# Performance work log

Measured on AMD Instinct MI355X. Metric: run time of the kernel, lower is better.

The kernel has to match this reference:

```python
import jax, jax.numpy as jnp
import numpy as np

N, E, F, H, C = 50000, 800000, 100, 128, 40
EPS = 1e-5


def setup_inputs() -> dict:
    key = jax.random.key(0)
    ks = jax.random.split(key, 9)
    s = 0.05
    return {
        "x": jax.random.normal(ks[0], (N, F), jnp.float32),
        "nbr": jax.random.normal(ks[1], (E, F), jnp.float32),
        "seg_ids": jnp.sort(jax.random.randint(ks[2], (E,), 0, N)),
        "W1x": jax.random.normal(ks[3], (H, F), jnp.float32) * s,
        "W1n": jax.random.normal(ks[4], (H, F), jnp.float32) * s,
        "g1": jnp.ones((), jnp.float32),
        "b1": jnp.zeros((), jnp.float32),
        "W2x": jax.random.normal(ks[5], (H, H), jnp.float32) * s,
        "W2n": jax.random.normal(ks[6], (H, H), jnp.float32) * s,
        "g2": jnp.ones((), jnp.float32),
        "b2": jnp.zeros((), jnp.float32),
        "Wc": jax.random.normal(ks[7], (C, H), jnp.float32) * s,
        "bc": jnp.zeros((C,), jnp.float32),
    }


def _seg_mean(v, ids, n):
    # ragged per-node neighbor mean: segment_sum / count
    s = jax.ops.segment_sum(v, ids, num_segments=n)
    cnt = jax.ops.segment_sum(jnp.ones((v.shape[0],), v.dtype), ids, num_segments=n)
    return s / jnp.maximum(cnt, 1.0)[:, None], cnt


def _bn_relu(t, g, b):
    # BatchNorm1d(1) in training mode on [N,1,d]: scalar mean/var over all elements
    m = t.mean()
    v = jnp.mean((t - m) ** 2)
    return jax.nn.relu(g * (t - m) * jax.lax.rsqrt(v + EPS) + b)


def _seg_bn_relu(nbr, ids, cnt, g, b, n):
    # BN applied per neighbor-list tensor: scalar stats per segment (over k_i * d elems)
    d = nbr.shape[1]
    ne = jnp.maximum(cnt * d, 1.0)
    sm = jax.ops.segment_sum(nbr.sum(axis=1), ids, num_segments=n) / ne
    sq = jax.ops.segment_sum((nbr * nbr).sum(axis=1), ids, num_segments=n) / ne
    var = sq - sm * sm
    inv = jax.lax.rsqrt(var + EPS)
    xn = (nbr - sm[ids, None]) * inv[ids, None]
    return jax.nn.relu(g * xn + b)


def reference(x, nbr, seg_ids, W1x, W1n, g1, b1, W2x, W2n, g2, b2, Wc, bc):
    n = x.shape[0]
    # layer 1: FeatTrans(feat_len -> hidden)
    f, cnt = _seg_mean(nbr, seg_ids, n)          # [N,F]
    h = x @ W1x.T + f @ W1n.T                    # [N,H]
    nbr1 = nbr @ W1x.T                           # [E,H]
    # acvt1
    h = _bn_relu(h, g1, b1)
    nbr1 = _seg_bn_relu(nbr1, seg_ids, cnt, g1, b1, n)
    # layer 2: FeatTrans(hidden -> hidden)
    f2, _ = _seg_mean(nbr1, seg_ids, n)          # [N,H]
    h = h @ W2x.T + f2 @ W2n.T                   # [N,H]
    # acvt2 + classifier
    h = _bn_relu(h, g2, b2)
    return h @ Wc.T + bc                         # [N,C]
```

## Files before the change

### kernel.cpp

```cpp
#include <hip/hip_runtime.h>
#include <hip/hip_bf16.h>
#include <math.h>

#define NN 50000
#define NE 800000
#define FD 100
#define HD 128
#define CD 40
#define EPSF 1e-5f
#define NTILE 6250
#define GRID_EDGE 512
#define NT_NODE 391

typedef __attribute__((ext_vector_type(8))) short short8;
typedef __attribute__((ext_vector_type(4))) float f32x4;

__device__ __forceinline__ unsigned short f2bf(float x) {
  union { __hip_bfloat16 h; unsigned short u; } cv;
  cv.h = __float2bfloat16(x);
  return cv.u;
}
__device__ __forceinline__ float bf2f(unsigned short b) {
  return __uint_as_float(((unsigned)b) << 16);
}

__device__ __forceinline__ void bar_lds() {
  asm volatile("s_waitcnt lgkmcnt(0)\n\ts_barrier" ::: "memory");
}

__global__ void k_rowptr(const int* __restrict__ seg, int* __restrict__ rp) {
  int i = blockIdx.x * blockDim.x + threadIdx.x;
  if (i > NN) return;
  int lo = 0, hi = NE;
  while (lo < hi) { int mid = (lo + hi) >> 1; if (seg[mid] < i) lo = mid + 1; else hi = mid; }
  rp[i] = lo;
}

__device__ __forceinline__ void cvt_write256(const float4* gv, char* rowbase, int q, int sr) {
  const float* vf = (const float*)gv;
#pragma unroll
  for (int h = 0; h < 4; ++h) {
    short8 s;
#pragma unroll
    for (int e = 0; e < 8; ++e) s[e] = (short)f2bf(vf[h * 8 + e]);
    *(short8*)(rowbase + ((q * 64 + h * 16) ^ ((sr & 7) << 4))) = s;
  }
}

__device__ __forceinline__ void load_quarters(const float* src, int q, float4* gv) {
#pragma unroll
  for (int i4 = 0; i4 < 8; ++i4) {
    const int c = q * 32 + i4 * 4;
    gv[i4] = (c < FD) ? *(const float4*)(src + c) : make_float4(0.f, 0.f, 0.f, 0.f);
  }
}

__global__ __launch_bounds__(512, 4) void k_gemm1(
    const float* __restrict__ nbr, const int* __restrict__ seg,
    const float* __restrict__ W1x,
    float* __restrict__ Ssum, float* __restrict__ Qsum, float* __restrict__ fsum) {
  __shared__ char lds[65536];
  __shared__ int segL[128];
  char* A = lds + 32768;
  const int tid = threadIdx.x;
  const int sr = tid >> 2, q = tid & 3;
  const int w = tid >> 6, l = tid & 63, lr = l & 15, lh = l >> 4;

  {
    float4 gv[8];
    load_quarters(W1x + (size_t)sr * FD, q, gv);
    cvt_write256(gv, lds + sr * 256, q, sr);
    load_quarters(nbr + (size_t)(blockIdx.x * 128 + sr) * FD, q, gv);
    cvt_write256(gv, A + sr * 256, q, sr);
    if (tid < 128) segL[tid] = seg[blockIdx.x * 128 + tid];
  }
  for (int t = blockIdx.x; t < NTILE; t += GRID_EDGE) {
    const int tn = t + GRID_EDGE;
    float4 gv[8];
    int sgn = 0;
    if (tn < NTILE) {
      load_quarters(nbr + (size_t)(tn * 128 + sr) * FD, q, gv);
      if (tid < 128) sgn = seg[tn * 128 + tid];
    }
    bar_lds();
    short8 af[4];
    const int arow = w * 16 + lr;
#pragma unroll
    for (int kk = 0; kk < 4; ++kk)
      af[kk] = *(const short8*)(A + arow * 256 + ((lh * 16 + kk * 64) ^ ((arow & 7) << 4)));

    float rs[4] = {0.f, 0.f, 0.f, 0.f}, rq[4] = {0.f, 0.f, 0.f, 0.f};
#pragma unroll
    for (int nt = 0; nt < 8; ++nt) {
      f32x4 acc = {0.f, 0.f, 0.f, 0.f};
#pragma unroll
      for (int kk = 0; kk < 4; ++kk) {
        const int n = nt * 16 + lr;
        const short8 bfg = *(const short8*)(lds + n * 256 + ((lh * 16 + kk * 64) ^ ((n & 7) << 4)));
        acc = __builtin_amdgcn_mfma_f32_16x16x32_bf16(af[kk], bfg, acc, 0, 0, 0);
      }
#pragma unroll
      for (int r = 0; r < 4; ++r) {
        const float val = acc[r];
        rs[r] += val;
        rq[r] = fmaf(val, val, rq[r]);
      }
    }
    float sv[4], qv[4];
#pragma unroll
    for (int r = 0; r < 4; ++r) {
      float a = rs[r], b = rq[r];
#pragma unroll
      for (int off = 1; off < 16; off <<= 1) { a += __shfl_xor(a, off); b += __shfl_xor(b, off); }
      sv[r] = a; qv[r] = b;
    }
    if (lr == 0) {
      const int R = w * 16 + lh * 4;
      const int4 nid = *(const int4*)&segL[R];
      float sa = sv[0], qa = qv[0];
      int curn = nid.x;
      if (nid.y != curn) { atomicAdd(&Ssum[curn], sa); atomicAdd(&Qsum[curn], qa); sa = 0.f; qa = 0.f; curn = nid.y; }
      sa += sv[1]; qa += qv[1];
      if (nid.z != curn) { atomicAdd(&Ssum[curn], sa); atomicAdd(&Qsum[curn], qa); sa = 0.f; qa = 0.f; curn = nid.z; }
      sa += sv[2]; qa += qv[2];
      if (nid.w != curn) { atomicAdd(&Ssum[curn], sa); atomicAdd(&Qsum[curn], qa); sa = 0.f; qa = 0.f; curn = nid.w; }
      sa += sv[3]; qa += qv[3];
      atomicAdd(&Ssum[curn], sa); atomicAdd(&Qsum[curn], qa);
    }
    {
      const int qq = tid >> 7, j = tid & 127;
      if (j < FD) {
        const int r0 = qq * 32;
        int curn = segL[r0];
        float acc = 0.f;
        bool inside = false;
#pragma unroll
        for (int b8 = 0; b8 < 4; ++b8) {
          float vals[8];
#pragma unroll
          for (int k = 0; k < 8; ++k) {
            const int row = r0 + b8 * 8 + k;
            vals[k] = bf2f(*(const unsigned short*)(A + row * 256 + ((j * 2) ^ ((row & 7) << 4))));
          }
#pragma unroll
          for (int k = 0; k < 8; ++k) {
            const int nd = segL[r0 + b8 * 8 + k];
            if (nd != curn) {
              float* dst = fsum + (size_t)curn * FD + j;
              if (inside) *dst = acc; else atomicAdd(dst, acc);
              inside = true; acc = 0.f; curn = nd;
            }
            acc += vals[k];
          }
        }
        atomicAdd(fsum + (size_t)curn * FD + j, acc);
      }
    }
    bar_lds();
    if (tn < NTILE) {
      cvt_write256(gv, A + sr * 256, q, sr);
      if (tid < 128) segL[tid] = sgn;
    }
  }
}

__global__ void k_nodestats(const int* __restrict__ rp, const float* __restrict__ Ssum,
                            const float* __restrict__ Qsum, float2* __restrict__ smi,
                            float* __restrict__ rcv) {
  const int i = blockIdx.x * blockDim.x + threadIdx.x;
  if (i >= NN) return;
  const int cnt = rp[i + 1] - rp[i];
  const float ne = fmaxf((float)cnt * (float)HD, 1.f);
  const float sm = Ssum[i] / ne;
  const float var = Qsum[i] / ne - sm * sm;
  smi[i] = make_float2(sm, rsqrtf(var + EPSF));
  rcv[i] = 1.f / (float)(cnt > 0 ? cnt : 1);
}

__global__ __launch_bounds__(512, 4) void k_fuse2(
    const float* __restrict__ nbr, const int* __restrict__ seg,
    const float* __restrict__ W1x, const float2* __restrict__ smi,
    const float* __restrict__ g1p, const float* __restrict__ b1p,
    float* __restrict__ f2sum) {
  __shared__ char lds[65536];
  __shared__ int segL[128];
  __shared__ float2 smrow[128];
  char* A = lds + 32768;
  const int tid = threadIdx.x;
  const int sr = tid >> 2, q = tid & 3;
  const int w = tid >> 6, l = tid & 63, lr = l & 15, lh = l >> 4;
  const float g1 = g1p[0], b1 = b1p[0];

  {
    float4 gv[8];
    load_quarters(W1x + (size_t)sr * FD, q, gv);
    cvt_write256(gv, lds + sr * 256, q, sr);
    load_quarters(nbr + (size_t)(blockIdx.x * 128 + sr) * FD, q, gv);
    cvt_write256(gv, A + sr * 256, q, sr);
    if (tid < 128) {
      const int nd = seg[blockIdx.x * 128 + tid];
      segL[tid] = nd;
      smrow[tid] = smi[nd];
    }
  }
  for (int t = blockIdx.x; t < NTILE; t += GRID_EDGE) {
    const int tn = t + GRID_EDGE;
    float4 gv[8];
    int sgn = 0;
    float2 smn = make_float2(0.f, 0.f);
    if (tn < NTILE) {
      load_quarters(nbr + (size_t)(tn * 128 + sr) * FD, q, gv);
      if (tid < 128) { sgn = seg[tn * 128 + tid]; smn = smi[sgn]; }
    }
    bar_lds();
    short8 af[4];
    const int arow = w * 16 + lr;
#pragma unroll
    for (int kk = 0; kk < 4; ++kk)
      af[kk] = *(const short8*)(A + arow * 256 + ((lh * 16 + kk * 64) ^ ((arow & 7) << 4)));
    float2 mi[4];
#pragma unroll
    for (int r = 0; r < 4; ++r) mi[r] = smrow[w * 16 + lh * 4 + r];
    bar_lds();
#pragma unroll
    for (int nt = 0; nt < 8; ++nt) {
      f32x4 acc = {0.f, 0.f, 0.f, 0.f};
#pragma unroll
      for (int kk = 0; kk < 4; ++kk) {
        const int n = nt * 16 + lr;
        const short8 bfg = *(const short8*)(lds + n * 256 + ((lh * 16 + kk * 64) ^ ((n & 7) << 4)));
        acc = __builtin_amdgcn_mfma_f32_16x16x32_bf16(af[kk], bfg, acc, 0, 0, 0);
      }
      const int col = nt * 16 + lr;
#pragma unroll
      for (int r = 0; r < 4; ++r) {
        const int row = w * 16 + lh * 4 + r;
        const float v = fmaxf(fmaf(g1, (acc[r] - mi[r].x) * mi[r].y, b1), 0.f);
        *(unsigned short*)(A + row * 256 + ((col * 2) ^ ((row & 7) << 4))) = f2bf(v);
      }
    }
    bar_lds();
    {
      const int qq = tid >> 7, j = tid & 127;
      const int r0 = qq * 32;
      int curn = segL[r0];
      float acc = 0.f;
      bool inside = false;
#pragma unroll
      for (int b8 = 0; b8 < 4; ++b8) {
        float vals[8];
#pragma unroll
        for (int k = 0; k < 8; ++k) {
          const int row = r0 + b8 * 8 + k;
          vals[k] = bf2f(*(const unsigned short*)(A + row * 256 + ((j * 2) ^ ((row & 7) << 4))));
        }
#pragma unroll
        for (int k = 0; k < 8; ++k) {
          const int nd = segL[r0 + b8 * 8 + k];
          if (nd != curn) {
            float* dst = f2sum + (size_t)curn * HD + j;
            if (inside) *dst = acc; else atomicAdd(dst, acc);
            inside = true; acc = 0.f; curn = nd;
          }
          acc += vals[k];
        }
      }
      atomicAdd(f2sum + (size_t)curn * HD + j, acc);
    }
    bar_lds();
    if (tn < NTILE) {
      cvt_write256(gv, A + sr * 256, q, sr);
      if (tid < 128) { segL[tid] = sgn; smrow[tid] = smn; }
    }
  }
}

template <bool L2>
__global__ __launch_bounds__(512) void k_ngemm(
    const float* __restrict__ P1, const float* __restrict__ P2,
    const float* __restrict__ rcv,
    const float* __restrict__ WA, const float* __restrict__ WB,
    const float* __restrict__ stats_in,
    const float* __restrict__ gp, const float* __restrict__ bp,
    float* __restrict__ out, float* __restrict__ so) {
  constexpr int KH = L2 ? HD : FD;
  __shared__ char lds[131072];
  __shared__ float sred[16];
  const int tid = threadIdx.x;
  float a1 = 1.f, c1 = 0.f;
  if (L2) {
    const float m = stats_in[0] * (1.f / ((float)NN * (float)HD));
    const float var = stats_in[1] * (1.f / ((float)NN * (float)HD)) - m * m;
    const float inv = rsqrtf(var + EPSF);
    a1 = gp[0] * inv; c1 = bp[0] - gp[0] * m * inv;
  }
  const int sr = tid >> 2, q = tid & 3;
  const bool half2 = (q >= 2);
  const int cbase = (q & 1) * 64;
  {
    const float* src = (half2 ? WB : WA) + (size_t)sr * KH;
    float v[64];
#pragma unroll
    for (int i4 = 0; i4 < 16; ++i4) {
      const int c = cbase + i4 * 4;
      float4 tv = make_float4(0.f, 0.f, 0.f, 0.f);
      if (c < KH) tv = *(const float4*)(src + c);
      v[i4 * 4 + 0] = tv.x; v[i4 * 4 + 1] = tv.y; v[i4 * 4 + 2] = tv.z; v[i4 * 4 + 3] = tv.w;
    }
    char* db = lds + 65536 + sr * 512;
#pragma unroll
    for (int h = 0; h < 8; ++h) {
      short8 s8;
#pragma unroll
      for (int e = 0; e < 8; ++e) s8[e] = (short)f2bf(v[h * 8 + e]);
      *(short8*)(db + ((q * 128 + h * 16) ^ ((sr & 7) << 4))) = s8;
    }
  }
  const int w = tid >> 6, l = tid & 63, lr = l & 15, lh = l >> 4;
  float ls = 0.f, lsq = 0.f;
  for (int bt = blockIdx.x; bt < NT_NODE; bt += gridDim.x) {
    __syncthreads();
    const size_t rg = (size_t)bt * 128 + sr;
    {
      const float* src = (half2 ? P2 : P1) + rg * KH;
      const float sc = half2 ? ((rg < NN) ? rcv[rg] : 0.f) : 1.f;
      float v[64];
#pragma unroll
      for (int i4 = 0; i4 < 16; ++i4) {
        const int c = cbase + i4 * 4;
        float4 tv = make_float4(0.f, 0.f, 0.f, 0.f);
        if (rg < NN && c < KH) tv = *(const float4*)(src + c);
        float e0 = tv.x, e1 = tv.y, e2 = tv.z, e3 = tv.w;
        if (half2) { e0 *= sc; e1 *= sc; e2 *= sc; e3 *= sc; }
        else if (L2 && rg < NN) {
          e0 = fmaxf(fmaf(a1, e0, c1), 0.f); e1 = fmaxf(fmaf(a1, e1, c1), 0.f);
          e2 = fmaxf(fmaf(a1, e2, c1), 0.f); e3 = fmaxf(fmaf(a1, e3, c1), 0.f);
        }
        v[i4 * 4 + 0] = e0; v[i4 * 4 + 1] = e1; v[i4 * 4 + 2] = e2; v[i4 * 4 + 3] = e3;
      }
      char* db = lds + sr * 512;
#pragma unroll
      for (int h = 0; h < 8; ++h) {
        short8 s8;
#pragma unroll
        for (int e = 0; e < 8; ++e) s8[e] = (short)f2bf(v[h * 8 + e]);
        *(short8*)(db + ((q * 128 + h * 16) ^ ((sr & 7) << 4))) = s8;
      }
    }
    __syncthreads();
    short8 af[8];
    const int arow = w * 16 + lr;
#pragma unroll
    for (int kk = 0; kk < 8; ++kk)
      af[kk] = *(const short8*)(lds + arow * 512 + ((lh * 16 + kk * 64) ^ ((arow & 7) << 4)));
    const char* B = lds + 65536;
#pragma unroll
    for (int nt = 0; nt < 8; ++nt) {
      f32x4 acc = {0.f, 0.f, 0.f, 0.f};
#pragma unroll
      for (int kk = 0; kk < 8; ++kk) {
        const int n = nt * 16 + lr;
        const short8 bfg = *(const short8*)(B + n * 512 + ((lh * 16 + kk * 64) ^ ((n & 7) << 4)));
        acc = __builtin_amdgcn_mfma_f32_16x16x32_bf16(af[kk], bfg, acc, 0, 0, 0);
      }
      const int col = nt * 16 + lr;
#pragma unroll
      for (int r = 0; r < 4; ++r) {
        const float val = acc[r];
        const size_t rg2 = (size_t)bt * 128 + w * 16 + lh * 4 + r;
        if (rg2 < NN) out[rg2 * HD + col] = val;
        ls += val;
        lsq = fmaf(val, val, lsq);
      }
    }
  }
#pragma unroll
  for (int off = 32; off > 0; off >>= 1) { ls += __shfl_down(ls, off); lsq += __shfl_down(lsq, off); }
  if ((tid & 63) == 0) { sred[(tid >> 6) * 2] = ls; sred[(tid >> 6) * 2 + 1] = lsq; }
  __syncthreads();
  if (tid == 0) {
    float S = 0.f, Q = 0.f;
#pragma unroll
    for (int i = 0; i < 8; ++i) { S += sred[i * 2]; Q += sred[i * 2 + 1]; }
    atomicAdd(&so[0], S);
    atomicAdd(&so[1], Q);
  }
}

__global__ __launch_bounds__(512) void k_cls(
    const float* __restrict__ h2, const float* __restrict__ Wc,
    const float* __restrict__ bc, const float* __restrict__ stats,
    const float* __restrict__ gp, const float* __restrict__ bp,
    float* __restrict__ out) {
  __shared__ char lds[45056];
  const int tid = threadIdx.x;
  const float m = stats[0] * (1.f / ((float)NN * (float)HD));
  const float var = stats[1] * (1.f / ((float)NN * (float)HD)) - m * m;
  const float inv = rsqrtf(var + EPSF);
  const float g = gp[0], bb = bp[0];
  const float a2 = g * inv, c2 = bb - g * m * inv;
  const int sr = tid >> 2, q = tid & 3;
  const size_t rg = (size_t)blockIdx.x * 128 + sr;
  {
    float4 gv[8];
#pragma unroll
    for (int i4 = 0; i4 < 8; ++i4) {
      const int c = q * 32 + i4 * 4;
      float4 t = (rg < NN) ? *(const float4*)(h2 + rg * HD + c) : make_float4(0.f, 0.f, 0.f, 0.f);
      t.x = fmaxf(fmaf(a2, t.x, c2), 0.f); t.y = fmaxf(fmaf(a2, t.y, c2), 0.f);
      t.z = fmaxf(fmaf(a2, t.z, c2), 0.f); t.w = fmaxf(fmaf(a2, t.w, c2), 0.f);
      gv[i4] = t;
    }
    cvt_write256(gv, lds + sr * 256, q, sr);
  }
  if (tid < 192) {
    const int bn = tid >> 2, bq = tid & 3;
    float4 gv[8];
#pragma unroll
    for (int i4 = 0; i4 < 8; ++i4) {
      const int c = bq * 32 + i4 * 4;
      gv[i4] = (bn < CD) ? *(const float4*)(Wc + (size_t)bn * HD + c) : make_float4(0.f, 0.f, 0.f, 0.f);
    }
    cvt_write256(gv, lds + 32768 + bn * 256, bq, bn);
  }
  __syncthreads();
  const int w = tid >> 6, l = tid & 63, lr = l & 15, lh = l >> 4;
  short8 af[4];
  const int arow = w * 16 + lr;
#pragma unroll
  for (int kk = 0; kk < 4; ++kk)
    af[kk] = *(const short8*)(lds + arow * 256 + ((lh * 16 + kk * 64) ^ ((arow & 7) << 4)));
#pragma unroll
  for (int nt = 0; nt < 3; ++nt) {
    f32x4 acc = {0.f, 0.f, 0.f, 0.f};
#pragma unroll
    for (int kk = 0; kk < 4; ++kk) {
      const int n = nt * 16 + lr;
      const short8 bfg = *(const short8*)(lds + 32768 + n * 256 + ((lh * 16 + kk * 64) ^ ((n & 7) << 4)));
      acc = __builtin_amdgcn_mfma_f32_16x16x32_bf16(af[kk], bfg, acc, 0, 0, 0);
    }
    const int col = nt * 16 + lr;
    if (col < CD) {
      const float bias = bc[col];
#pragma unroll
      for (int r = 0; r < 4; ++r) {
        const size_t rg2 = (size_t)blockIdx.x * 128 + w * 16 + lh * 4 + r;
        if (rg2 < NN) out[rg2 * CD + col] = acc[r] + bias;
      }
    }
  }
}

extern "C" void kernel_launch(void* const* d_in, const int* in_sizes, int n_in,
                              void* d_out, int out_size, void* d_ws, size_t ws_size,
                              hipStream_t stream) {
  const float* x   = (const float*)d_in[0];
  const float* nbr = (const float*)d_in[1];
  const int*   seg = (const int*)d_in[2];
  const float* W1x = (const float*)d_in[3];
  const float* W1n = (const float*)d_in[4];
  const float* g1  = (const float*)d_in[5];
  const float* b1  = (const float*)d_in[6];
  const float* W2x = (const float*)d_in[7];
  const float* W2n = (const float*)d_in[8];
  const float* g2  = (const float*)d_in[9];
  const float* b2  = (const float*)d_in[10];
  const float* Wc  = (const float*)d_in[11];
  const float* bc  = (const float*)d_in[12];
  float* out = (float*)d_out;

  char* p = (char*)d_ws;
  auto alloc = [&](size_t bytes) {
    char* q = p;
    p += (bytes + 255) & ~(size_t)255;
    return q;
  };
  int*    rp    = (int*)   alloc(sizeof(int) * (NN + 1));
  float*  fsum  = (float*) alloc(sizeof(float) * (size_t)NN * FD);
  float*  f2sum = (float*) alloc(sizeof(float) * (size_t)NN * HD);
  float*  hpre  = (float*) alloc(sizeof(float) * (size_t)NN * HD);
  float*  h2    = (float*) alloc(sizeof(float) * (size_t)NN * HD);
  float*  stats = (float*) alloc(sizeof(float) * 4);
  float*  Ssum  = (float*) alloc(sizeof(float) * (size_t)NN);
  float*  Qsum  = (float*) alloc(sizeof(float) * (size_t)NN);
  float2* smi   = (float2*)alloc(sizeof(float2) * (size_t)NN);
  float*  rcv   = (float*) alloc(sizeof(float) * (size_t)NN);

  hipMemsetAsync(stats, 0, sizeof(float) * 4, stream);
  hipMemsetAsync(fsum, 0, sizeof(float) * (size_t)NN * FD, stream);
  hipMemsetAsync(f2sum, 0, sizeof(float) * (size_t)NN * HD, stream);
  hipMemsetAsync(Ssum, 0, sizeof(float) * (size_t)NN, stream);
  hipMemsetAsync(Qsum, 0, sizeof(float) * (size_t)NN, stream);

  k_rowptr<<<(NN + 256) / 256, 256, 0, stream>>>(seg, rp);
  k_gemm1<<<GRID_EDGE, 512, 0, stream>>>(nbr, seg, W1x, Ssum, Qsum, fsum);
  k_nodestats<<<(NN + 255) / 256, 256, 0, stream>>>(rp, Ssum, Qsum, smi, rcv);
  k_fuse2<<<GRID_EDGE, 512, 0, stream>>>(nbr, seg, W1x, smi, g1, b1, f2sum);
  k_ngemm<false><<<256, 512, 0, stream>>>(x, fsum, rcv, W1x, W1n, stats, g1, b1, hpre, stats);
  k_ngemm<true><<<256, 512, 0, stream>>>(hpre, f2sum, rcv, W2x, W2n, stats, g1, b1, h2, stats + 2);
  k_cls<<<NT_NODE, 512, 0, stream>>>(h2, Wc, bc, stats + 2, g2, b2, out);
}
```

Measured before the change: 425.9 us.

## Double-buffer edge tiles and keep W1x fragments in registers in edge kernels

The two edge kernels now keep the W1x B-fragments in registers for the whole kernel instead of re-reading them from LDS every tile. The A tile and segment/stat buffers are double-buffered, with the next tile written into the alternate buffer during the current iteration, which removes one barrier per iteration. The grid is halved and the occupancy hint is dropped, because register and LDS use per block grow. This risks lower occupancy and less latency hiding from fewer waves.

```diff
diff --git a/kernel.cpp b/kernel.cpp
--- a/kernel.cpp
+++ b/kernel.cpp
@@ -9,7 +9,7 @@
 #define CD 40
 #define EPSF 1e-5f
 #define NTILE 6250
-#define GRID_EDGE 512
+#define GRID_EDGE 256
 #define NT_NODE 391
 
 typedef __attribute__((ext_vector_type(8))) short short8;
@@ -55,25 +55,36 @@
   }
 }
 
-__global__ __launch_bounds__(512, 4) void k_gemm1(
+__global__ __launch_bounds__(512) void k_gemm1(
     const float* __restrict__ nbr, const int* __restrict__ seg,
     const float* __restrict__ W1x,
     float* __restrict__ Ssum, float* __restrict__ Qsum, float* __restrict__ fsum) {
   __shared__ char lds[65536];
-  __shared__ int segL[128];
-  char* A = lds + 32768;
+  __shared__ int segL[2][128];
   const int tid = threadIdx.x;
   const int sr = tid >> 2, q = tid & 3;
   const int w = tid >> 6, l = tid & 63, lr = l & 15, lh = l >> 4;
 
+  short8 bfr[8][4];
   {
     float4 gv[8];
     load_quarters(W1x + (size_t)sr * FD, q, gv);
     cvt_write256(gv, lds + sr * 256, q, sr);
+    __syncthreads();
+#pragma unroll
+    for (int nt = 0; nt < 8; ++nt) {
+#pragma unroll
+      for (int kk = 0; kk < 4; ++kk) {
+        const int n = nt * 16 + lr;
+        bfr[nt][kk] = *(const short8*)(lds + n * 256 + ((lh * 16 + kk * 64) ^ ((n & 7) << 4)));
+      }
+    }
+    __syncthreads();
     load_quarters(nbr + (size_t)(blockIdx.x * 128 + sr) * FD, q, gv);
-    cvt_write256(gv, A + sr * 256, q, sr);
-    if (tid < 128) segL[tid] = seg[blockIdx.x * 128 + tid];
-  }
+    cvt_write256(gv, lds + sr * 256, q, sr);
+    if (tid < 128) segL[0][tid] = seg[blockIdx.x * 128 + tid];
+  }
+  int cur = 0;
   for (int t = blockIdx.x; t < NTILE; t += GRID_EDGE) {
     const int tn = t + GRID_EDGE;
     float4 gv[8];
@@ -83,6 +94,7 @@
       if (tid < 128) sgn = seg[tn * 128 + tid];
     }
     bar_lds();
+    const char* A = lds + cur * 32768;
     short8 af[4];
     const int arow = w * 16 + lr;
 #pragma unroll
@@ -94,11 +106,8 @@
     for (int nt = 0; nt < 8; ++nt) {
       f32x4 acc = {0.f, 0.f, 0.f, 0.f};
 #pragma unroll
-      for (int kk = 0; kk < 4; ++kk) {
-        const int n = nt * 16 + lr;
-        const short8 bfg = *(const short8*)(lds + n * 256 + ((lh * 16 + kk * 64) ^ ((n & 7) << 4)));
-        acc = __builtin_amdgcn_mfma_f32_16x16x32_bf16(af[kk], bfg, acc, 0, 0, 0);
-      }
+      for (int kk = 0; kk < 4; ++kk)
+        acc = __builtin_amdgcn_mfma_f32_16x16x32_bf16(af[kk], bfr[nt][kk], acc, 0, 0, 0);
 #pragma unroll
       for (int r = 0; r < 4; ++r) {
         const float val = acc[r];
@@ -116,7 +125,7 @@
     }
     if (lr == 0) {
       const int R = w * 16 + lh * 4;
-      const int4 nid = *(const int4*)&segL[R];
+      const int4 nid = *(const int4*)&segL[cur][R];
       float sa = sv[0], qa = qv[0];
       int curn = nid.x;
       if (nid.y != curn) { atomicAdd(&Ssum[curn], sa); atomicAdd(&Qsum[curn], qa); sa = 0.f; qa = 0.f; curn = nid.y; }
@@ -127,11 +136,16 @@
       sa += sv[3]; qa += qv[3];
       atomicAdd(&Ssum[curn], sa); atomicAdd(&Qsum[curn], qa);
     }
+    if (tn < NTILE) {
+      cvt_write256(gv, lds + (cur ^ 1) * 32768 + sr * 256, q, sr);
+      if (tid < 128) segL[cur ^ 1][tid] = sgn;
+    }
     {
       const int qq = tid >> 7, j = tid & 127;
       if (j < FD) {
         const int r0 = qq * 32;
-        int curn = segL[r0];
+        const int* sl = segL[cur];
+        int curn = sl[r0];
         float acc = 0.f;
         bool inside = false;
 #pragma unroll
@@ -144,7 +158,7 @@
           }
 #pragma unroll
           for (int k = 0; k < 8; ++k) {
-            const int nd = segL[r0 + b8 * 8 + k];
+            const int nd = sl[r0 + b8 * 8 + k];
             if (nd != curn) {
               float* dst = fsum + (size_t)curn * FD + j;
               if (inside) *dst = acc; else atomicAdd(dst, acc);
@@ -156,11 +170,7 @@
         atomicAdd(fsum + (size_t)curn * FD + j, acc);
       }
     }
-    bar_lds();
-    if (tn < NTILE) {
-      cvt_write256(gv, A + sr * 256, q, sr);
-      if (tid < 128) segL[tid] = sgn;
-    }
+    cur ^= 1;
   }
 }
 
@@ -177,32 +187,44 @@
   rcv[i] = 1.f / (float)(cnt > 0 ? cnt : 1);
 }
 
-__global__ __launch_bounds__(512, 4) void k_fuse2(
+__global__ __launch_bounds__(512) void k_fuse2(
     const float* __restrict__ nbr, const int* __restrict__ seg,
     const float* __restrict__ W1x, const float2* __restrict__ smi,
     const float* __restrict__ g1p, const float* __restrict__ b1p,
     float* __restrict__ f2sum) {
-  __shared__ char lds[65536];
-  __shared__ int segL[128];
-  __shared__ float2 smrow[128];
-  char* A = lds + 32768;
+  __shared__ char lds[98304];
+  __shared__ int segL[2][128];
+  __shared__ float2 smrow[2][128];
+  char* P = lds + 65536;
   const int tid = threadIdx.x;
   const int sr = tid >> 2, q = tid & 3;
   const int w = tid >> 6, l = tid & 63, lr = l & 15, lh = l >> 4;
   const float g1 = g1p[0], b1 = b1p[0];
 
+  short8 bfr[8][4];
   {
     float4 gv[8];
     load_quarters(W1x + (size_t)sr * FD, q, gv);
     cvt_write256(gv, lds + sr * 256, q, sr);
+    __syncthreads();
+#pragma unroll
+    for (int nt = 0; nt < 8; ++nt) {
+#pragma unroll
+      for (int kk = 0; kk < 4; ++kk) {
+        const int n = nt * 16 + lr;
+        bfr[nt][kk] = *(const short8*)(lds + n * 256 + ((lh * 16 + kk * 64) ^ ((n & 7) << 4)));
+      }
+    }
+    __syncthreads();
     load_quarters(nbr + (size_t)(blockIdx.x * 128 + sr) * FD, q, gv);
-    cvt_write256(gv, A + sr * 256, q, sr);
+    cvt_write256(gv, lds + sr * 256, q, sr);
     if (tid < 128) {
       const int nd = seg[blockIdx.x * 128 + tid];
-      segL[tid] = nd;
-      smrow[tid] = smi[nd];
-    }
-  }
+      segL[0][tid] = nd;
+      smrow[0][tid] = smi[nd];
+    }
+  }
+  int cur = 0;
   for (int t = blockIdx.x; t < NTILE; t += GRID_EDGE) {
     const int tn = t + GRID_EDGE;
     float4 gv[8];
@@ -213,6 +235,7 @@
       if (tid < 128) { sgn = seg[tn * 128 + tid]; smn = smi[sgn]; }
     }
     bar_lds();
+    const char* A = lds + cur * 32768;
     short8 af[4];
     const int arow = w * 16 + lr;
 #pragma unroll
@@ -220,30 +243,31 @@
       af[kk] = *(const short8*)(A + arow * 256 + ((lh * 16 + kk * 64) ^ ((arow & 7) << 4)));
     float2 mi[4];
 #pragma unroll
-    for (int r = 0; r < 4; ++r) mi[r] = smrow[w * 16 + lh * 4 + r];
-    bar_lds();
+    for (int r = 0; r < 4; ++r) mi[r] = smrow[cur][w * 16 + lh * 4 + r];
 #pragma unroll
     for (int nt = 0; nt < 8; ++nt) {
       f32x4 acc = {0.f, 0.f, 0.f, 0.f};
 #pragma unroll
-      for (int kk = 0; kk < 4; ++kk) {
-        const int n = nt * 16 + lr;
-        const short8 bfg = *(const short8*)(lds + n * 256 + ((lh * 16 + kk * 64) ^ ((n & 7) << 4)));
-        acc = __builtin_amdgcn_mfma_f32_16x16x32_bf16(af[kk], bfg, acc, 0, 0, 0);
-      }
+      for (int kk = 0; kk < 4; ++kk)
+        acc = __builtin_amdgcn_mfma_f32_16x16x32_bf16(af[kk], bfr[nt][kk], acc, 0, 0, 0);
       const int col = nt * 16 + lr;
 #pragma unroll
       for (int r = 0; r < 4; ++r) {
         const int row = w * 16 + lh * 4 + r;
         const float v = fmaxf(fmaf(g1, (acc[r] - mi[r].x) * mi[r].y, b1), 0.f);
-        *(unsigned short*)(A + row * 256 + ((col * 2) ^ ((row & 7) << 4))) = f2bf(v);
-      }
+        *(unsigned short*)(P + row * 256 + ((col * 2) ^ ((row & 7) << 4))) = f2bf(v);
+      }
+    }
+    if (tn < NTILE) {
+      cvt_write256(gv, lds + (cur ^ 1) * 32768 + sr * 256, q, sr);
+      if (tid < 128) { segL[cur ^ 1][tid] = sgn; smrow[cur ^ 1][tid] = smn; }
     }
     bar_lds();
     {
       const int qq = tid >> 7, j = tid & 127;
       const int r0 = qq * 32;
-      int curn = segL[r0];
+      const int* sl = segL[cur];
+      int curn = sl[r0];
       float acc = 0.f;
       bool inside = false;
 #pragma unroll
@@ -252,11 +276,11 @@
 #pragma unroll
         for (int k = 0; k < 8; ++k) {
           const int row = r0 + b8 * 8 + k;
-          vals[k] = bf2f(*(const unsigned short*)(A + row * 256 + ((j * 2) ^ ((row & 7) << 4))));
+          vals[k] = bf2f(*(const unsigned short*)(P + row * 256 + ((j * 2) ^ ((row & 7) << 4))));
         }
 #pragma unroll
         for (int k = 0; k < 8; ++k) {
-          const int nd = segL[r0 + b8 * 8 + k];
+          const int nd = sl[r0 + b8 * 8 + k];
           if (nd != curn) {
             float* dst = f2sum + (size_t)curn * HD + j;
             if (inside) *dst = acc; else atomicAdd(dst, acc);
@@ -267,11 +291,7 @@
       }
       atomicAdd(f2sum + (size_t)curn * HD + j, acc);
     }
-    bar_lds();
-    if (tn < NTILE) {
-      cvt_write256(gv, A + sr * 256, q, sr);
-      if (tid < 128) { segL[tid] = sgn; smrow[tid] = smn; }
-    }
+    cur ^= 1;
   }
 }
 
```

Result: slower. 460.5 us (+8.1%).
